# Kernel tuning notes

Measured on AMD Instinct MI355X. Metric: run time of the kernel, lower is better.

Reference implementation:

```python
import jax, jax.numpy as jnp
import numpy as np

MAX_FEATURES = 5000
EMBED_DIM = 100
H1, H2, NUM_CLASSES = 64, 32, 4
BATCH, SEQ = 1024, 256


def _keras_lstm_scan(x_seq, mask_seq, W, U, b):
    """x_seq: [T,B,E], mask_seq: [T,B] bool. Keras gate order i,f,c,o.
    Masked steps carry (h, c) through unchanged (Keras mask_zero semantics).
    Returns (all hidden states [T,B,H], final hidden [B,H])."""
    B = x_seq.shape[1]
    H = U.shape[0]
    h0 = jnp.zeros((B, H), x_seq.dtype)
    c0 = jnp.zeros((B, H), x_seq.dtype)

    def step(carry, inp):
        h, c = carry
        x, m = inp
        z = x @ W + h @ U + b  # [B, 4H]
        i, f, g, o = jnp.split(z, 4, axis=-1)
        i = jax.nn.sigmoid(i)
        f = jax.nn.sigmoid(f)
        g = jnp.tanh(g)
        o = jax.nn.sigmoid(o)
        c_new = f * c + i * g
        h_new = o * jnp.tanh(c_new)
        m = m[:, None]
        h2 = jnp.where(m, h_new, h)
        c2 = jnp.where(m, c_new, c)
        return (h2, c2), h2

    (hT, _), hs = jax.lax.scan(step, (h0, c0), (x_seq, mask_seq))
    return hs, hT


def setup_inputs() -> dict:
    key = jax.random.key(0)
    ks = jax.random.split(key, 8)
    s = 0.05
    tokens = jax.random.randint(ks[0], (BATCH, SEQ), 0, MAX_FEATURES, dtype=jnp.int32)
    emb = jax.random.normal(ks[1], (MAX_FEATURES, EMBED_DIM), jnp.float32) * s
    W1 = jax.random.normal(ks[2], (EMBED_DIM, 4 * H1), jnp.float32) * s
    U1 = jax.random.normal(ks[3], (H1, 4 * H1), jnp.float32) * s
    b1 = jnp.zeros((4 * H1,), jnp.float32)
    W2 = jax.random.normal(ks[4], (H1, 4 * H2), jnp.float32) * s
    U2 = jax.random.normal(ks[5], (H2, 4 * H2), jnp.float32) * s
    b2 = jnp.zeros((4 * H2,), jnp.float32)
    Wd = jax.random.normal(ks[6], (H2, NUM_CLASSES), jnp.float32) * s
    bd = jnp.zeros((NUM_CLASSES,), jnp.float32)
    return {"tokens": tokens, "emb": emb, "W1": W1, "U1": U1, "b1": b1,
            "W2": W2, "U2": U2, "b2": b2, "Wd": Wd, "bd": bd}


def reference(tokens, emb, W1, U1, b1, W2, U2, b2, Wd, bd):
    mask = (tokens != 0)                       # [B,T] mask_zero=True
    x = emb[tokens]                            # [B,T,E]
    x_t = jnp.transpose(x, (1, 0, 2))          # [T,B,E]
    m_t = jnp.transpose(mask, (1, 0))          # [T,B]
    hs1, _ = _keras_lstm_scan(x_t, m_t, W1, U1, b1)   # [T,B,64]
    _, h2 = _keras_lstm_scan(hs1, m_t, W2, U2, b2)    # [B,32] last valid state
    return jax.nn.sigmoid(h2 @ Wd + bd)        # [B,4]
```

## Files before the change

kernel.cpp:

```cpp
#include <hip/hip_runtime.h>

typedef _Float16 hp2 __attribute__((ext_vector_type(2)));

#define NB    1024
#define TT    256
#define EE    100
#define VOCAB 5000
#define GG1   256
#define GG2   128

__device__ __forceinline__ float fast_sigmoid(float x) {
  return __builtin_amdgcn_rcpf(1.0f + __expf(-x));
}
__device__ __forceinline__ float fast_tanh(float x) {
  return 1.0f - 2.0f * __builtin_amdgcn_rcpf(1.0f + __expf(2.0f * x));
}

__device__ __forceinline__ void step_sync() {
  asm volatile("s_waitcnt lgkmcnt(0)" ::: "memory");
  __builtin_amdgcn_s_barrier();
  __builtin_amdgcn_sched_barrier(0);
}

__global__ __launch_bounds__(256) void emb_gemm(
    const float* __restrict__ emb, const float* __restrict__ W1,
    const float* __restrict__ b1, float* __restrict__ emb_zi)
{
  __shared__ float sE[8][EE];
  const int j  = threadIdx.x;
  const int v0 = blockIdx.x * 8;
  for (int idx = j; idx < 8 * EE; idx += 256) {
    int r = idx / EE, k = idx % EE;
    sE[r][k] = emb[(size_t)(v0 + r) * EE + k];
  }
  __syncthreads();
  float acc[8];
  const float bb = b1[j];
  #pragma unroll
  for (int r = 0; r < 8; ++r) acc[r] = bb;
  for (int k = 0; k < EE; ++k) {
    float w = W1[k * GG1 + j];
    #pragma unroll
    for (int r = 0; r < 8; ++r) acc[r] = fmaf(sE[r][k], w, acc[r]);
  }
  const int slot = (j & 63) * 4 + (j >> 6);
  #pragma unroll
  for (int r = 0; r < 8; ++r) emb_zi[(size_t)(v0 + r) * GG1 + slot] = acc[r];
}

__global__ __launch_bounds__(128) __attribute__((amdgpu_waves_per_eu(2, 2)))
void lstm_dual(
    const int* __restrict__ tokens, const float* __restrict__ emb_zi,
    const float* __restrict__ U1,
    const float* __restrict__ W2, const float* __restrict__ U2, const float* __restrict__ b2,
    const float* __restrict__ Wd, const float* __restrict__ bd,
    float* __restrict__ out)
{
  __shared__ __align__(16) _Float16 sHB[2][96];
  __shared__ int sTok[TT];

  const int tid = threadIdx.x;
  const int u   = tid & 63;
  const int wv  = tid >> 6;
  const int row = blockIdx.x;

  ((int2*)sTok)[tid] = ((const int2*)(tokens + (size_t)row * TT))[tid];
  if (tid < 96) { sHB[0][tid] = (_Float16)0.0f; sHB[1][tid] = (_Float16)0.0f; }

  if (wv == 0) {
    hp2 wA[128];
    #pragma unroll
    for (int p = 0; p < 32; ++p) {
      #pragma unroll
      for (int g = 0; g < 4; ++g) {
        hp2 w;
        w[0] = (_Float16)U1[(2 * p + 0) * GG1 + g * 64 + u];
        w[1] = (_Float16)U1[(2 * p + 1) * GG1 + g * 64 + u];
        wA[4 * p + g] = w;
      }
    }
    __syncthreads();

    float c1 = 0.f, h1r = 0.f;
    {
      int tok0 = sTok[0];
      float4 zx0 = *(const float4*)&emb_zi[(size_t)tok0 * GG1 + 4 * u];
      if (tok0 != 0) {
        float iv = fast_sigmoid(zx0.x);
        float gv = fast_tanh(zx0.z);
        float ov = fast_sigmoid(zx0.w);
        c1 = iv * gv; h1r = ov * fast_tanh(c1);
      }
      sHB[0][u] = (_Float16)h1r;
    }
    int   tok_a = sTok[1];
    float4 zxa = *(const float4*)&emb_zi[(size_t)tok_a * GG1 + 4 * u];
    step_sync();

    for (int t = 0; t < TT; ++t) {
      if (t + 1 < TT) {
        float a0 = zxa.x, a1 = zxa.y, a2 = zxa.z, a3 = zxa.w;
        int tok_n = 0;
        if (t + 2 < TT) {
          tok_n = sTok[t + 2];
          zxa = *(const float4*)&emb_zi[(size_t)tok_n * GG1 + 4 * u];
        }
        const int4* rb = (const int4*)&sHB[t & 1][0];
        #pragma unroll
        for (int q = 0; q < 8; ++q) {
          int4 hq = rb[q];
          #pragma unroll
          for (int pp = 0; pp < 4; ++pp) {
            const int p = 4 * q + pp;
            hp2 hv = ((const hp2*)&hq)[pp];
            a0 = __builtin_amdgcn_fdot2(hv, wA[4 * p + 0], a0, false);
            a1 = __builtin_amdgcn_fdot2(hv, wA[4 * p + 1], a1, false);
            a2 = __builtin_amdgcn_fdot2(hv, wA[4 * p + 2], a2, false);
            a3 = __builtin_amdgcn_fdot2(hv, wA[4 * p + 3], a3, false);
          }
        }
        {
          const bool ma = (tok_a != 0);
          float iv = fast_sigmoid(a0);
          float fv = fast_sigmoid(a1);
          float gv = fast_tanh(a2);
          float ov = fast_sigmoid(a3);
          if (ma) { c1 = fv * c1 + iv * gv; h1r = ov * fast_tanh(c1); }
        }
        sHB[(t & 1) ^ 1][u] = (_Float16)h1r;
        tok_a = tok_n;
      }
      step_sync();
    }
  } else {
    const int u2 = u & 31;
    const int s  = u >> 5;
    hp2 wB[96];
    #pragma unroll
    for (int p = 0; p < 24; ++p) {
      int k0 = 48 * s + 2 * p;
      const float* r0 = (k0     < 64) ? &W2[(size_t)k0 * GG2]       : &U2[(size_t)(k0 - 64) * GG2];
      const float* r1 = (k0 + 1 < 64) ? &W2[(size_t)(k0 + 1) * GG2] : &U2[(size_t)(k0 + 1 - 64) * GG2];
      #pragma unroll
      for (int g = 0; g < 4; ++g) {
        hp2 w;
        w[0] = (_Float16)r0[g * 32 + u2];
        w[1] = (_Float16)r1[g * 32 + u2];
        wB[4 * p + g] = w;
      }
    }
    const float bi2 = b2[u2], bf2 = b2[32 + u2], bg2 = b2[64 + u2], bo2 = b2[96 + u2];
    __syncthreads();

    float c2 = 0.f, h2r = 0.f;
    step_sync();

    for (int t = 0; t < TT; ++t) {
      const int tok_b = sTok[t];
      float b0 = 0.f, b1v = 0.f, b2v = 0.f, b3 = 0.f;
      const int4* hbp = (const int4*)(&sHB[t & 1][48 * s]);
      #pragma unroll
      for (int q = 0; q < 6; ++q) {
        int4 hq = hbp[q];
        #pragma unroll
        for (int pp = 0; pp < 4; ++pp) {
          const int p = 4 * q + pp;
          hp2 hv = ((const hp2*)&hq)[pp];
          b0  = __builtin_amdgcn_fdot2(hv, wB[4 * p + 0], b0,  false);
          b1v = __builtin_amdgcn_fdot2(hv, wB[4 * p + 1], b1v, false);
          b2v = __builtin_amdgcn_fdot2(hv, wB[4 * p + 2], b2v, false);
          b3  = __builtin_amdgcn_fdot2(hv, wB[4 * p + 3], b3,  false);
        }
      }
      b0  += __shfl_xor(b0, 32);
      b1v += __shfl_xor(b1v, 32);
      b2v += __shfl_xor(b2v, 32);
      b3  += __shfl_xor(b3, 32);
      {
        const bool mb = (tok_b != 0);
        float i2 = fast_sigmoid(b0 + bi2);
        float f2 = fast_sigmoid(b1v + bf2);
        float g2 = fast_tanh(b2v + bg2);
        float o2 = fast_sigmoid(b3 + bo2);
        if (mb) { c2 = f2 * c2 + i2 * g2; h2r = o2 * fast_tanh(c2); }
      }
      if (s == 0) sHB[(t & 1) ^ 1][64 + u2] = (_Float16)h2r;
      step_sync();
    }
  }
  __syncthreads();

  if (tid < 4) {
    float a = bd[tid];
    #pragma unroll
    for (int k = 0; k < 32; ++k)
      a = fmaf((float)sHB[0][64 + k], Wd[k * 4 + tid], a);
    out[(size_t)row * 4 + tid] = fast_sigmoid(a);
  }
}

extern "C" void kernel_launch(void* const* d_in, const int* in_sizes, int n_in,
                              void* d_out, int out_size, void* d_ws, size_t ws_size,
                              hipStream_t stream) {
  const int*   tokens = (const int*)d_in[0];
  const float* emb    = (const float*)d_in[1];
  const float* W1     = (const float*)d_in[2];
  const float* U1     = (const float*)d_in[3];
  const float* b1     = (const float*)d_in[4];
  const float* W2     = (const float*)d_in[5];
  const float* U2     = (const float*)d_in[6];
  const float* b2     = (const float*)d_in[7];
  const float* Wd     = (const float*)d_in[8];
  const float* bd     = (const float*)d_in[9];
  float* out    = (float*)d_out;
  float* emb_zi = (float*)d_ws;

  emb_gemm<<<dim3(VOCAB / 8), dim3(256), 0, stream>>>(emb, W1, b1, emb_zi);
  lstm_dual<<<dim3(NB), dim3(128), 0, stream>>>(
      tokens, emb_zi, U1, W2, U2, b2, Wd, bd, out);
}
```

Before: 223.1 us.

## Split each LSTM layer across two waves with cross-lane reduction

The per-row recurrent kernel grows from two waves to four: each layer now uses two waves, and each lane computes a partial dot product over half (layer 1) or a quarter (layer 2) of the reduction dimension. The partials are combined with xor shuffles. This shortens the serial dot-product chain per timestep, which sits on the recurrence critical path. In exchange the block is larger, each step pays extra shuffle latency, and more waves have to pass the per-step barrier.

```diff
diff --git a/kernel.cpp b/kernel.cpp
--- a/kernel.cpp
+++ b/kernel.cpp
@@ -48,8 +48,8 @@
   for (int r = 0; r < 8; ++r) emb_zi[(size_t)(v0 + r) * GG1 + slot] = acc[r];
 }
 
-__global__ __launch_bounds__(128) __attribute__((amdgpu_waves_per_eu(2, 2)))
-void lstm_dual(
+__global__ __launch_bounds__(256) __attribute__((amdgpu_waves_per_eu(4, 4)))
+void lstm_quad(
     const int* __restrict__ tokens, const float* __restrict__ emb_zi,
     const float* __restrict__ U1,
     const float* __restrict__ W2, const float* __restrict__ U2, const float* __restrict__ b2,
@@ -60,22 +60,26 @@
   __shared__ int sTok[TT];
 
   const int tid = threadIdx.x;
-  const int u   = tid & 63;
+  const int l   = tid & 63;
   const int wv  = tid >> 6;
   const int row = blockIdx.x;
 
-  ((int2*)sTok)[tid] = ((const int2*)(tokens + (size_t)row * TT))[tid];
+  if (tid < 128) ((int2*)sTok)[tid] = ((const int2*)(tokens + (size_t)row * TT))[tid];
   if (tid < 96) { sHB[0][tid] = (_Float16)0.0f; sHB[1][tid] = (_Float16)0.0f; }
 
-  if (wv == 0) {
-    hp2 wA[128];
-    #pragma unroll
-    for (int p = 0; p < 32; ++p) {
+  if (wv < 2) {
+    const int ul = l & 31;
+    const int s  = l >> 5;
+    const int u  = 32 * wv + ul;
+    hp2 wA[64];
+    #pragma unroll
+    for (int p = 0; p < 16; ++p) {
+      int k0 = 32 * s + 2 * p;
       #pragma unroll
       for (int g = 0; g < 4; ++g) {
         hp2 w;
-        w[0] = (_Float16)U1[(2 * p + 0) * GG1 + g * 64 + u];
-        w[1] = (_Float16)U1[(2 * p + 1) * GG1 + g * 64 + u];
+        w[0] = (_Float16)U1[(k0 + 0) * GG1 + g * 64 + u];
+        w[1] = (_Float16)U1[(k0 + 1) * GG1 + g * 64 + u];
         wA[4 * p + g] = w;
       }
     }
@@ -91,7 +95,7 @@
         float ov = fast_sigmoid(zx0.w);
         c1 = iv * gv; h1r = ov * fast_tanh(c1);
       }
-      sHB[0][u] = (_Float16)h1r;
+      if (s == 0) sHB[0][u] = (_Float16)h1r;
     }
     int   tok_a = sTok[1];
     float4 zxa = *(const float4*)&emb_zi[(size_t)tok_a * GG1 + 4 * u];
@@ -99,15 +103,16 @@
 
     for (int t = 0; t < TT; ++t) {
       if (t + 1 < TT) {
-        float a0 = zxa.x, a1 = zxa.y, a2 = zxa.z, a3 = zxa.w;
         int tok_n = 0;
+        float4 zxn = zxa;
         if (t + 2 < TT) {
           tok_n = sTok[t + 2];
-          zxa = *(const float4*)&emb_zi[(size_t)tok_n * GG1 + 4 * u];
-        }
-        const int4* rb = (const int4*)&sHB[t & 1][0];
+          zxn = *(const float4*)&emb_zi[(size_t)tok_n * GG1 + 4 * u];
+        }
+        float a0 = 0.f, a1 = 0.f, a2 = 0.f, a3 = 0.f;
+        const int4* rb = (const int4*)&sHB[t & 1][32 * s];
         #pragma unroll
-        for (int q = 0; q < 8; ++q) {
+        for (int q = 0; q < 4; ++q) {
           int4 hq = rb[q];
           #pragma unroll
           for (int pp = 0; pp < 4; ++pp) {
@@ -119,26 +124,30 @@
             a3 = __builtin_amdgcn_fdot2(hv, wA[4 * p + 3], a3, false);
           }
         }
+        a0 += __shfl_xor(a0, 32);
+        a1 += __shfl_xor(a1, 32);
+        a2 += __shfl_xor(a2, 32);
+        a3 += __shfl_xor(a3, 32);
         {
           const bool ma = (tok_a != 0);
-          float iv = fast_sigmoid(a0);
-          float fv = fast_sigmoid(a1);
-          float gv = fast_tanh(a2);
-          float ov = fast_sigmoid(a3);
+          float iv = fast_sigmoid(a0 + zxa.x);
+          float fv = fast_sigmoid(a1 + zxa.y);
+          float gv = fast_tanh(a2 + zxa.z);
+          float ov = fast_sigmoid(a3 + zxa.w);
           if (ma) { c1 = fv * c1 + iv * gv; h1r = ov * fast_tanh(c1); }
         }
-        sHB[(t & 1) ^ 1][u] = (_Float16)h1r;
-        tok_a = tok_n;
+        if (s == 0) sHB[(t & 1) ^ 1][u] = (_Float16)h1r;
+        tok_a = tok_n; zxa = zxn;
       }
       step_sync();
     }
   } else {
-    const int u2 = u & 31;
-    const int s  = u >> 5;
-    hp2 wB[96];
-    #pragma unroll
-    for (int p = 0; p < 24; ++p) {
-      int k0 = 48 * s + 2 * p;
+    const int u2 = 16 * (wv - 2) + (l & 15);
+    const int ss = l >> 4;
+    hp2 wB[48];
+    #pragma unroll
+    for (int p = 0; p < 12; ++p) {
+      int k0 = 24 * ss + 2 * p;
       const float* r0 = (k0     < 64) ? &W2[(size_t)k0 * GG2]       : &U2[(size_t)(k0 - 64) * GG2];
       const float* r1 = (k0 + 1 < 64) ? &W2[(size_t)(k0 + 1) * GG2] : &U2[(size_t)(k0 + 1 - 64) * GG2];
       #pragma unroll
@@ -158,9 +167,9 @@
     for (int t = 0; t < TT; ++t) {
       const int tok_b = sTok[t];
       float b0 = 0.f, b1v = 0.f, b2v = 0.f, b3 = 0.f;
-      const int4* hbp = (const int4*)(&sHB[t & 1][48 * s]);
+      const int4* hbp = (const int4*)(&sHB[t & 1][24 * ss]);
       #pragma unroll
-      for (int q = 0; q < 6; ++q) {
+      for (int q = 0; q < 3; ++q) {
         int4 hq = hbp[q];
         #pragma unroll
         for (int pp = 0; pp < 4; ++pp) {
@@ -172,10 +181,10 @@
           b3  = __builtin_amdgcn_fdot2(hv, wB[4 * p + 3], b3,  false);
         }
       }
-      b0  += __shfl_xor(b0, 32);
-      b1v += __shfl_xor(b1v, 32);
-      b2v += __shfl_xor(b2v, 32);
-      b3  += __shfl_xor(b3, 32);
+      b0  += __shfl_xor(b0, 16);  b0  += __shfl_xor(b0, 32);
+      b1v += __shfl_xor(b1v, 16); b1v += __shfl_xor(b1v, 32);
+      b2v += __shfl_xor(b2v, 16); b2v += __shfl_xor(b2v, 32);
+      b3  += __shfl_xor(b3, 16);  b3  += __shfl_xor(b3, 32);
       {
         const bool mb = (tok_b != 0);
         float i2 = fast_sigmoid(b0 + bi2);
@@ -184,7 +193,7 @@
         float o2 = fast_sigmoid(b3 + bo2);
         if (mb) { c2 = f2 * c2 + i2 * g2; h2r = o2 * fast_tanh(c2); }
       }
-      if (s == 0) sHB[(t & 1) ^ 1][64 + u2] = (_Float16)h2r;
+      if (ss == 0) sHB[(t & 1) ^ 1][64 + u2] = (_Float16)h2r;
       step_sync();
     }
   }
@@ -216,6 +225,6 @@
   float* emb_zi = (float*)d_ws;
 
   emb_gemm<<<dim3(VOCAB / 8), dim3(256), 0, stream>>>(emb, W1, b1, emb_zi);
-  lstm_dual<<<dim3(NB), dim3(128), 0, stream>>>(
+  lstm_quad<<<dim3(NB), dim3(256), 0, stream>>>(
       tokens, emb_zi, U1, W2, U2, b2, Wd, bd, out);
 }
```

Result: slower. 272.3 us (+22.0%).

## Pipeline LSTM layers in chunks with full layer-1 history in LDS

Applied to the files above, without the earlier changes.

Layer 1's hidden states now go into a full per-timestep history buffer in LDS instead of a double buffer. This lets the two wavefronts sync once per 8-step chunk rather than every timestep, with layer 2 running one chunk behind layer 1. Within a chunk, each wave relies on intra-wave ordering and a compiler memory fence only. Inline asm pins the weight registers. This cuts block-wide barriers by about 8x, at the cost of 32KB more LDS and a small extra pipeline latency of one chunk.

```diff
diff --git a/kernel.cpp b/kernel.cpp
--- a/kernel.cpp
+++ b/kernel.cpp
@@ -8,6 +8,8 @@
 #define VOCAB 5000
 #define GG1   256
 #define GG2   128
+#define CHK   8
+#define NCH   (TT / CHK)
 
 __device__ __forceinline__ float fast_sigmoid(float x) {
   return __builtin_amdgcn_rcpf(1.0f + __expf(-x));
@@ -16,10 +18,13 @@
   return 1.0f - 2.0f * __builtin_amdgcn_rcpf(1.0f + __expf(2.0f * x));
 }
 
-__device__ __forceinline__ void step_sync() {
+__device__ __forceinline__ void chunk_sync() {
   asm volatile("s_waitcnt lgkmcnt(0)" ::: "memory");
   __builtin_amdgcn_s_barrier();
   __builtin_amdgcn_sched_barrier(0);
+}
+__device__ __forceinline__ void lds_fence() {
+  asm volatile("" ::: "memory");
 }
 
 __global__ __launch_bounds__(256) void emb_gemm(
@@ -49,14 +54,15 @@
 }
 
 __global__ __launch_bounds__(128) __attribute__((amdgpu_waves_per_eu(2, 2)))
-void lstm_dual(
+void lstm_pipe(
     const int* __restrict__ tokens, const float* __restrict__ emb_zi,
     const float* __restrict__ U1,
     const float* __restrict__ W2, const float* __restrict__ U2, const float* __restrict__ b2,
     const float* __restrict__ Wd, const float* __restrict__ bd,
     float* __restrict__ out)
 {
-  __shared__ __align__(16) _Float16 sHB[2][96];
+  __shared__ __align__(16) _Float16 hist1[TT][64];
+  __shared__ __align__(16) _Float16 h2buf[32];
   __shared__ int sTok[TT];
 
   const int tid = threadIdx.x;
@@ -65,7 +71,7 @@
   const int row = blockIdx.x;
 
   ((int2*)sTok)[tid] = ((const int2*)(tokens + (size_t)row * TT))[tid];
-  if (tid < 96) { sHB[0][tid] = (_Float16)0.0f; sHB[1][tid] = (_Float16)0.0f; }
+  if (tid < 32) h2buf[tid] = (_Float16)0.0f;
 
   if (wv == 0) {
     hp2 wA[128];
@@ -79,6 +85,12 @@
         wA[4 * p + g] = w;
       }
     }
+    #define PIN16(B) asm volatile("" : "+v"(wA[B+0]),"+v"(wA[B+1]),"+v"(wA[B+2]),"+v"(wA[B+3]),\
+      "+v"(wA[B+4]),"+v"(wA[B+5]),"+v"(wA[B+6]),"+v"(wA[B+7]),"+v"(wA[B+8]),"+v"(wA[B+9]),\
+      "+v"(wA[B+10]),"+v"(wA[B+11]),"+v"(wA[B+12]),"+v"(wA[B+13]),"+v"(wA[B+14]),"+v"(wA[B+15]))
+    PIN16(0); PIN16(16); PIN16(32); PIN16(48);
+    PIN16(64); PIN16(80); PIN16(96); PIN16(112);
+    #undef PIN16
     __syncthreads();
 
     float c1 = 0.f, h1r = 0.f;
@@ -91,46 +103,57 @@
         float ov = fast_sigmoid(zx0.w);
         c1 = iv * gv; h1r = ov * fast_tanh(c1);
       }
-      sHB[0][u] = (_Float16)h1r;
-    }
-    int   tok_a = sTok[1];
-    float4 zxa = *(const float4*)&emb_zi[(size_t)tok_a * GG1 + 4 * u];
-    step_sync();
-
-    for (int t = 0; t < TT; ++t) {
-      if (t + 1 < TT) {
-        float a0 = zxa.x, a1 = zxa.y, a2 = zxa.z, a3 = zxa.w;
-        int tok_n = 0;
-        if (t + 2 < TT) {
-          tok_n = sTok[t + 2];
-          zxa = *(const float4*)&emb_zi[(size_t)tok_n * GG1 + 4 * u];
+      hist1[0][u] = (_Float16)h1r;
+      lds_fence();
+    }
+    int   tokA = sTok[1];
+    float4 zxA = *(const float4*)&emb_zi[(size_t)tokA * GG1 + 4 * u];
+    int   tokB = sTok[2];
+    float4 zxB = *(const float4*)&emb_zi[(size_t)tokB * GG1 + 4 * u];
+
+    for (int c = 0; c <= NCH; ++c) {
+      if (c < NCH) {
+        #pragma unroll
+        for (int tt = 0; tt < CHK; ++tt) {
+          const int t = CHK * c + tt;
+          if (t == 0) continue;
+          float4 zc; int tokc;
+          if (t & 1) { zc = zxA; tokc = tokA; }
+          else       { zc = zxB; tokc = tokB; }
+          if (t + 2 < TT) {
+            int tok_n = sTok[t + 2];
+            float4 zn = *(const float4*)&emb_zi[(size_t)tok_n * GG1 + 4 * u];
+            if (t & 1) { zxA = zn; tokA = tok_n; }
+            else       { zxB = zn; tokB = tok_n; }
+          }
+          float a0 = 0.f, a1 = 0.f, a2 = 0.f, a3 = 0.f;
+          const int4* rb = (const int4*)&hist1[t - 1][0];
+          #pragma unroll
+          for (int q = 0; q < 8; ++q) {
+            int4 hq = rb[q];
+            #pragma unroll
+            for (int pp = 0; pp < 4; ++pp) {
+              const int p = 4 * q + pp;
+              hp2 hv = ((const hp2*)&hq)[pp];
+              a0 = __builtin_amdgcn_fdot2(hv, wA[4 * p + 0], a0, false);
+              a1 = __builtin_amdgcn_fdot2(hv, wA[4 * p + 1], a1, false);
+              a2 = __builtin_amdgcn_fdot2(hv, wA[4 * p + 2], a2, false);
+              a3 = __builtin_amdgcn_fdot2(hv, wA[4 * p + 3], a3, false);
+            }
+          }
+          {
+            const bool ma = (tokc != 0);
+            float iv = fast_sigmoid(a0 + zc.x);
+            float fv = fast_sigmoid(a1 + zc.y);
+            float gv = fast_tanh(a2 + zc.z);
+            float ov = fast_sigmoid(a3 + zc.w);
+            if (ma) { c1 = fv * c1 + iv * gv; h1r = ov * fast_tanh(c1); }
+          }
+          hist1[t][u] = (_Float16)h1r;
+          lds_fence();
         }
-        const int4* rb = (const int4*)&sHB[t & 1][0];
-        #pragma unroll
-        for (int q = 0; q < 8; ++q) {
-          int4 hq = rb[q];
-          #pragma unroll
-          for (int pp = 0; pp < 4; ++pp) {
-            const int p = 4 * q + pp;
-            hp2 hv = ((const hp2*)&hq)[pp];
-            a0 = __builtin_amdgcn_fdot2(hv, wA[4 * p + 0], a0, false);
-            a1 = __builtin_amdgcn_fdot2(hv, wA[4 * p + 1], a1, false);
-            a2 = __builtin_amdgcn_fdot2(hv, wA[4 * p + 2], a2, false);
-            a3 = __builtin_amdgcn_fdot2(hv, wA[4 * p + 3], a3, false);
-          }
-        }
-        {
-          const bool ma = (tok_a != 0);
-          float iv = fast_sigmoid(a0);
-          float fv = fast_sigmoid(a1);
-          float gv = fast_tanh(a2);
-          float ov = fast_sigmoid(a3);
-          if (ma) { c1 = fv * c1 + iv * gv; h1r = ov * fast_tanh(c1); }
-        }
-        sHB[(t & 1) ^ 1][u] = (_Float16)h1r;
-        tok_a = tok_n;
-      }
-      step_sync();
+      }
+      chunk_sync();
     }
   } else {
     const int u2 = u & 31;
@@ -149,43 +172,55 @@
         wB[4 * p + g] = w;
       }
     }
+    #define PIN16B(B) asm volatile("" : "+v"(wB[B+0]),"+v"(wB[B+1]),"+v"(wB[B+2]),"+v"(wB[B+3]),\
+      "+v"(wB[B+4]),"+v"(wB[B+5]),"+v"(wB[B+6]),"+v"(wB[B+7]),"+v"(wB[B+8]),"+v"(wB[B+9]),\
+      "+v"(wB[B+10]),"+v"(wB[B+11]),"+v"(wB[B+12]),"+v"(wB[B+13]),"+v"(wB[B+14]),"+v"(wB[B+15]))
+    PIN16B(0); PIN16B(16); PIN16B(32); PIN16B(48); PIN16B(64); PIN16B(80);
+    #undef PIN16B
     const float bi2 = b2[u2], bf2 = b2[32 + u2], bg2 = b2[64 + u2], bo2 = b2[96 + u2];
     __syncthreads();
 
     float c2 = 0.f, h2r = 0.f;
-    step_sync();
-
-    for (int t = 0; t < TT; ++t) {
-      const int tok_b = sTok[t];
-      float b0 = 0.f, b1v = 0.f, b2v = 0.f, b3 = 0.f;
-      const int4* hbp = (const int4*)(&sHB[t & 1][48 * s]);
-      #pragma unroll
-      for (int q = 0; q < 6; ++q) {
-        int4 hq = hbp[q];
+    for (int c = 0; c <= NCH; ++c) {
+      if (c >= 1) {
+        const int cc = c - 1;
         #pragma unroll
-        for (int pp = 0; pp < 4; ++pp) {
-          const int p = 4 * q + pp;
-          hp2 hv = ((const hp2*)&hq)[pp];
-          b0  = __builtin_amdgcn_fdot2(hv, wB[4 * p + 0], b0,  false);
-          b1v = __builtin_amdgcn_fdot2(hv, wB[4 * p + 1], b1v, false);
-          b2v = __builtin_amdgcn_fdot2(hv, wB[4 * p + 2], b2v, false);
-          b3  = __builtin_amdgcn_fdot2(hv, wB[4 * p + 3], b3,  false);
+        for (int tt = 0; tt < CHK; ++tt) {
+          const int t = CHK * cc + tt;
+          const int tok_b = sTok[t];
+          float b0 = 0.f, b1v = 0.f, b2v = 0.f, b3 = 0.f;
+          #pragma unroll
+          for (int q = 0; q < 6; ++q) {
+            const int k0 = 48 * s + 8 * q;
+            const _Float16* src = (k0 < 64) ? &hist1[t][k0] : &h2buf[k0 - 64];
+            int4 hq = *(const int4*)src;
+            #pragma unroll
+            for (int pp = 0; pp < 4; ++pp) {
+              const int p = 4 * q + pp;
+              hp2 hv = ((const hp2*)&hq)[pp];
+              b0  = __builtin_amdgcn_fdot2(hv, wB[4 * p + 0], b0,  false);
+              b1v = __builtin_amdgcn_fdot2(hv, wB[4 * p + 1], b1v, false);
+              b2v = __builtin_amdgcn_fdot2(hv, wB[4 * p + 2], b2v, false);
+              b3  = __builtin_amdgcn_fdot2(hv, wB[4 * p + 3], b3,  false);
+            }
+          }
+          b0  += __shfl_xor(b0, 32);
+          b1v += __shfl_xor(b1v, 32);
+          b2v += __shfl_xor(b2v, 32);
+          b3  += __shfl_xor(b3, 32);
+          {
+            const bool mb = (tok_b != 0);
+            float i2 = fast_sigmoid(b0 + bi2);
+            float f2 = fast_sigmoid(b1v + bf2);
+            float g2 = fast_tanh(b2v + bg2);
+            float o2 = fast_sigmoid(b3 + bo2);
+            if (mb) { c2 = f2 * c2 + i2 * g2; h2r = o2 * fast_tanh(c2); }
+          }
+          if (s == 0) h2buf[u2] = (_Float16)h2r;
+          lds_fence();
         }
       }
-      b0  += __shfl_xor(b0, 32);
-      b1v += __shfl_xor(b1v, 32);
-      b2v += __shfl_xor(b2v, 32);
-      b3  += __shfl_xor(b3, 32);
-      {
-        const bool mb = (tok_b != 0);
-        float i2 = fast_sigmoid(b0 + bi2);
-        float f2 = fast_sigmoid(b1v + bf2);
-        float g2 = fast_tanh(b2v + bg2);
-        float o2 = fast_sigmoid(b3 + bo2);
-        if (mb) { c2 = f2 * c2 + i2 * g2; h2r = o2 * fast_tanh(c2); }
-      }
-      if (s == 0) sHB[(t & 1) ^ 1][64 + u2] = (_Float16)h2r;
-      step_sync();
+      chunk_sync();
     }
   }
   __syncthreads();
@@ -194,7 +229,7 @@
     float a = bd[tid];
     #pragma unroll
     for (int k = 0; k < 32; ++k)
-      a = fmaf((float)sHB[0][64 + k], Wd[k * 4 + tid], a);
+      a = fmaf((float)h2buf[k], Wd[k * 4 + tid], a);
     out[(size_t)row * 4 + tid] = fast_sigmoid(a);
   }
 }
@@ -216,6 +251,6 @@
   float* emb_zi = (float*)d_ws;
 
   emb_gemm<<<dim3(VOCAB / 8), dim3(256), 0, stream>>>(emb, W1, b1, emb_zi);
-  lstm_dual<<<dim3(NB), dim3(128), 0, stream>>>(
+  lstm_pipe<<<dim3(NB), dim3(128), 0, stream>>>(
       tokens, emb_zi, U1, W2, U2, b2, Wd, bd, out);
 }
```

Result: slower. 230.5 us (+3.3%).
